# Kernel optimization log

Measured on AMD Instinct MI355X. Metric: run time of the kernel, lower is better.

The kernel has to match this reference:

```python
import jax, jax.numpy as jnp
import numpy as np

DEG = 7
RANK = 8
B = 2_000_000

def setup_inputs() -> dict:
    key = jax.random.key(0)
    k_x, k0, k1, k2, k3 = jax.random.split(key, 5)
    d1 = DEG + 1
    # xavier_normal std = sqrt(2 / (fan_in + fan_out)); for 3D cores torch uses
    # fan_in = rank*(deg+1) style flattening, but any gaussian init is fine for a
    # numerical reference; use std matching 2D xavier on the (first, last) dims.
    def xavier(k, shape):
        fan_in, fan_out = shape[0], shape[-1]
        std = np.sqrt(2.0 / (fan_in + fan_out))
        return jax.random.normal(k, shape, dtype=jnp.float32) * std
    return {
        "X": jax.random.normal(k_x, (B, 4), dtype=jnp.float32),
        "G0": xavier(k0, (d1, RANK)),
        "G1": xavier(k1, (RANK, d1, RANK)),
        "G2": xavier(k2, (RANK, d1, RANK)),
        "G3": xavier(k3, (RANK, d1)),
    }

def reference(X, G0, G1, G2, G3):
    # poly bases: P[b, dim, p] = X[b, dim] ** p, p = 0..deg
    exps = jnp.arange(DEG + 1)               # [d1]
    P = X[:, :, None] ** exps                # [B, 4, d1]
    # chained TT contraction, left to right (avoids any large intermediate)
    t = jnp.einsum('bd,dr->br', P[:, 0], G0)           # [B, r]
    t = jnp.einsum('br,rds,bd->bs', t, G1, P[:, 1])    # [B, r]
    t = jnp.einsum('bs,sdt,bd->bt', t, G2, P[:, 2])    # [B, r]
    res = jnp.einsum('bt,td,bd->b', t, G3, P[:, 3])    # [B]
    return res.reshape(-1, 1)
```

## Files before the change

kernel.cpp:

```cpp
#include <hip/hip_runtime.h>
#include <hip/hip_bf16.h>

typedef float f32x4 __attribute__((ext_vector_type(4)));
typedef short bf16x8 __attribute__((ext_vector_type(8)));

__device__ inline unsigned cvt_pk_bf16(float a, float b) {
    unsigned r;
    asm("v_cvt_pk_bf16_f32 %0, %1, %2" : "=v"(r) : "v"(a), "v"(b));
    return r;
}
union FragU { unsigned u[4]; bf16x8 v; };

__device__ inline bf16x8 pack8(const float f[8]) {
    FragU x;
    x.u[0] = cvt_pk_bf16(f[0], f[1]);
    x.u[1] = cvt_pk_bf16(f[2], f[3]);
    x.u[2] = cvt_pk_bf16(f[4], f[5]);
    x.u[3] = cvt_pk_bf16(f[6], f[7]);
    return x.v;
}

__device__ inline bf16x8 splat8(float v) {
    FragU x;
    unsigned p = cvt_pk_bf16(v, v);
    x.u[0] = p; x.u[1] = p; x.u[2] = p; x.u[3] = p;
    return x.v;
}

__device__ inline void wave_fence() {
    asm volatile("s_waitcnt lgkmcnt(0)" ::: "memory");
    __builtin_amdgcn_sched_barrier(0);
}

__device__ inline void build_b(const float* __restrict__ G, int col, int grp,
                               bf16x8* Bh, bf16x8* Bl) {
    #pragma unroll
    for (int q = 0; q < 2; ++q) {
        FragU hi, lo;
        #pragma unroll
        for (int pr = 0; pr < 4; ++pr) {
            float v0 = 0.f, v1 = 0.f;
            if (col < 8) {
                v0 = G[(32*q + 8*grp + 2*pr    ) * 8 + col];
                v1 = G[(32*q + 8*grp + 2*pr + 1) * 8 + col];
            }
            float h0 = __bfloat162float(__float2bfloat16(v0));
            float h1 = __bfloat162float(__float2bfloat16(v1));
            hi.u[pr] = cvt_pk_bf16(h0, h1);
            lo.u[pr] = cvt_pk_bf16(v0 - h0, v1 - h1);
        }
        Bh[q] = hi.v;
        Bl[q] = lo.v;
    }
}

#define POWERS(p, xx)                                              \
    p[0] = 1.f;  p[1] = (xx);      p[2] = p[1]*p[1];               \
    p[3] = p[2]*p[1]; p[4] = p[2]*p[2]; p[5] = p[4]*p[1];          \
    p[6] = p[4]*p[2]; p[7] = p[4]*p[3];

#define ROWW 12

__global__ __launch_bounds__(256) void tt_poly_kernel(
    const float* __restrict__ X,
    const float* __restrict__ G0,
    const float* __restrict__ G1,
    const float* __restrict__ G2,
    const float* __restrict__ G3,
    float* __restrict__ out,
    int B, int NW)
{
    __shared__ float L[4][3][64 * ROWW];

    const int tid  = threadIdx.x;
    const int w    = tid >> 6;
    const int lane = tid & 63;
    const int col  = lane & 15;
    const int grp  = lane >> 4;

    int rowLbl[4], slotLbl[4], colOk[4];
    {
        bf16x8 ones = splat8(1.f);
        bf16x8 lbl  = splat8((float)col);
        f32x4 pr = {0.f, 0.f, 0.f, 0.f};
        f32x4 pc = {0.f, 0.f, 0.f, 0.f};
        pr = __builtin_amdgcn_mfma_f32_16x16x32_bf16(lbl, ones, pr, 0, 0, 0);
        pc = __builtin_amdgcn_mfma_f32_16x16x32_bf16(ones, lbl, pc, 0, 0, 0);
        #pragma unroll
        for (int j = 0; j < 4; ++j) {
            rowLbl[j] = (int)(pr[j] * 0.03125f + 0.5f);
            int c     = (int)(pc[j] * 0.03125f + 0.5f);
            colOk[j]  = (c < 8);
            slotLbl[j] = 2 * (c & 3) + ((c >> 2) & 1);
        }
    }

    bf16x8 B1h[2], B1l[2], B2h[2], B2l[2];
    build_b(G1, col, grp, B1h, B1l);
    build_b(G2, col, grp, B2h, B2l);

    float* T0 = &L[w][0][0];
    float* T1 = &L[w][1][0];
    float* T2 = &L[w][2][0];
    const int gw = blockIdx.x * 4 + w;

    #pragma unroll 1
    for (int it = 0; it < 4; ++it) {
        const int b = (it * NW + gw) * 64 + lane;
        float4 xv = make_float4(0.f, 0.f, 0.f, 0.f);
        if (b < B) xv = reinterpret_cast<const float4*>(X)[b];

        {
            float p[8];
            POWERS(p, xv.x)
            float t[8];
            #pragma unroll
            for (int r = 0; r < 8; ++r) {
                float a = 0.f;
                #pragma unroll
                for (int d = 0; d < 8; ++d)
                    a = fmaf(p[d], G0[d*8 + r], a);
                t[r] = a;
            }
            f32x4 v0 = {t[0], t[4], t[1], t[5]};
            f32x4 v1 = {t[2], t[6], t[3], t[7]};
            *reinterpret_cast<f32x4*>(&T0[lane*ROWW    ]) = v0;
            *reinterpret_cast<f32x4*>(&T0[lane*ROWW + 4]) = v1;
            *reinterpret_cast<float2*>(&T0[lane*ROWW + 8]) = make_float2(xv.y, xv.z);
        }
        wave_fence();

        #pragma unroll
        for (int g4 = 0; g4 < 4; ++g4) {
            const int base = (g4*16 + col) * ROWW;
            float2 tp = *reinterpret_cast<const float2*>(&T0[base + 2*grp]);
            float x1  = T0[base + 8];
            float p[8];
            POWERS(p, x1)
            float f0[8], f1[8];
            #pragma unroll
            for (int e = 0; e < 8; ++e) { f0[e] = tp.x*p[e]; f1[e] = tp.y*p[e]; }
            bf16x8 a0 = pack8(f0), a1 = pack8(f1);
            f32x4 acc = {0.f, 0.f, 0.f, 0.f};
            acc = __builtin_amdgcn_mfma_f32_16x16x32_bf16(a0, B1h[0], acc, 0, 0, 0);
            acc = __builtin_amdgcn_mfma_f32_16x16x32_bf16(a0, B1l[0], acc, 0, 0, 0);
            acc = __builtin_amdgcn_mfma_f32_16x16x32_bf16(a1, B1h[1], acc, 0, 0, 0);
            acc = __builtin_amdgcn_mfma_f32_16x16x32_bf16(a1, B1l[1], acc, 0, 0, 0);
            #pragma unroll
            for (int j = 0; j < 4; ++j)
                if (colOk[j])
                    T1[(g4*16 + rowLbl[j])*ROWW + slotLbl[j]] = acc[j];
        }
        wave_fence();

        #pragma unroll
        for (int g4 = 0; g4 < 4; ++g4) {
            const int base = (g4*16 + col) * ROWW;
            float2 tp = *reinterpret_cast<const float2*>(&T1[base + 2*grp]);
            float x2  = T0[base + 9];
            float p[8];
            POWERS(p, x2)
            float f0[8], f1[8];
            #pragma unroll
            for (int e = 0; e < 8; ++e) { f0[e] = tp.x*p[e]; f1[e] = tp.y*p[e]; }
            bf16x8 a0 = pack8(f0), a1 = pack8(f1);
            f32x4 acc = {0.f, 0.f, 0.f, 0.f};
            acc = __builtin_amdgcn_mfma_f32_16x16x32_bf16(a0, B2h[0], acc, 0, 0, 0);
            acc = __builtin_amdgcn_mfma_f32_16x16x32_bf16(a0, B2l[0], acc, 0, 0, 0);
            acc = __builtin_amdgcn_mfma_f32_16x16x32_bf16(a1, B2h[1], acc, 0, 0, 0);
            acc = __builtin_amdgcn_mfma_f32_16x16x32_bf16(a1, B2l[1], acc, 0, 0, 0);
            #pragma unroll
            for (int j = 0; j < 4; ++j)
                if (colOk[j])
                    T2[(g4*16 + rowLbl[j])*ROWW + slotLbl[j]] = acc[j];
        }
        wave_fence();

        {
            f32x4 u0 = *reinterpret_cast<const f32x4*>(&T2[lane*ROWW    ]);
            f32x4 u1 = *reinterpret_cast<const f32x4*>(&T2[lane*ROWW + 4]);
            const int tmap[8] = {0, 4, 1, 5, 2, 6, 3, 7};
            float p[8];
            POWERS(p, xv.w)
            float res = 0.f;
            #pragma unroll
            for (int sl = 0; sl < 8; ++sl) {
                const int t8 = tmap[sl];
                float wt = G3[t8*8];
                #pragma unroll
                for (int d = 1; d < 8; ++d)
                    wt = fmaf(p[d], G3[t8*8 + d], wt);
                float tv = (sl < 4) ? u0[sl] : u1[sl - 4];
                res = fmaf(tv, wt, res);
            }
            if (b < B) out[b] = res;
        }
    }
}

extern "C" void kernel_launch(void* const* d_in, const int* in_sizes, int n_in,
                              void* d_out, int out_size, void* d_ws, size_t ws_size,
                              hipStream_t stream) {
    const float* X  = (const float*)d_in[0];
    const float* G0 = (const float*)d_in[1];
    const float* G1 = (const float*)d_in[2];
    const float* G2 = (const float*)d_in[3];
    const float* G3 = (const float*)d_in[4];
    float* out = (float*)d_out;

    int B = in_sizes[0] / 4;
    int block = 256;
    int grid = (B + 1023) / 1024;
    int NW = grid * 4;
    tt_poly_kernel<<<grid, block, 0, stream>>>(X, G0, G1, G2, G3, out, B, NW);
}
```

Measured before the change: 40.37 us.

## Fold G0 into G1 core and restructure LDS staging with vectorized stores

Precomputes G0·G1 into a combined MFMA B operand, so the first contraction builds the x0 powers directly in the A fragment and the per-sample 64-FMA G0 stage and its LDS round trip are gone. LDS intermediates move to a transposed [slot][sample] layout that takes whole f32x4 stores when the MFMA lane mapping matches the expected one, with a scalar fallback otherwise. All four X loads are hoisted ahead of the loop and the loop is fully unrolled to overlap global latency. This costs extra registers and per-block setup FMAs, and the fused core may change rounding in the split-bf16 path.

```diff
diff --git a/kernel.cpp b/kernel.cpp
--- a/kernel.cpp
+++ b/kernel.cpp
@@ -11,7 +11,7 @@
 }
 union FragU { unsigned u[4]; bf16x8 v; };
 
-__device__ inline bf16x8 pack8(const float f[8]) {
+__device__ inline bf16x8 pack8(const float* f) {
     FragU x;
     x.u[0] = cvt_pk_bf16(f[0], f[1]);
     x.u[1] = cvt_pk_bf16(f[2], f[3]);
@@ -19,39 +19,15 @@
     x.u[3] = cvt_pk_bf16(f[6], f[7]);
     return x.v;
 }
-
 __device__ inline bf16x8 splat8(float v) {
     FragU x;
     unsigned p = cvt_pk_bf16(v, v);
     x.u[0] = p; x.u[1] = p; x.u[2] = p; x.u[3] = p;
     return x.v;
 }
-
 __device__ inline void wave_fence() {
     asm volatile("s_waitcnt lgkmcnt(0)" ::: "memory");
     __builtin_amdgcn_sched_barrier(0);
-}
-
-__device__ inline void build_b(const float* __restrict__ G, int col, int grp,
-                               bf16x8* Bh, bf16x8* Bl) {
-    #pragma unroll
-    for (int q = 0; q < 2; ++q) {
-        FragU hi, lo;
-        #pragma unroll
-        for (int pr = 0; pr < 4; ++pr) {
-            float v0 = 0.f, v1 = 0.f;
-            if (col < 8) {
-                v0 = G[(32*q + 8*grp + 2*pr    ) * 8 + col];
-                v1 = G[(32*q + 8*grp + 2*pr + 1) * 8 + col];
-            }
-            float h0 = __bfloat162float(__float2bfloat16(v0));
-            float h1 = __bfloat162float(__float2bfloat16(v1));
-            hi.u[pr] = cvt_pk_bf16(h0, h1);
-            lo.u[pr] = cvt_pk_bf16(v0 - h0, v1 - h1);
-        }
-        Bh[q] = hi.v;
-        Bl[q] = lo.v;
-    }
 }
 
 #define POWERS(p, xx)                                              \
@@ -59,7 +35,7 @@
     p[3] = p[2]*p[1]; p[4] = p[2]*p[2]; p[5] = p[4]*p[1];          \
     p[6] = p[4]*p[2]; p[7] = p[4]*p[3];
 
-#define ROWW 12
+#define TS 72
 
 __global__ __launch_bounds__(256) void tt_poly_kernel(
     const float* __restrict__ X,
@@ -70,15 +46,27 @@
     float* __restrict__ out,
     int B, int NW)
 {
-    __shared__ float L[4][3][64 * ROWW];
+    __shared__ float Xb[4][256];
+    __shared__ float T1s[4][8 * TS];
+    __shared__ float T2s[4][8 * TS];
 
     const int tid  = threadIdx.x;
     const int w    = tid >> 6;
     const int lane = tid & 63;
     const int col  = lane & 15;
     const int grp  = lane >> 4;
-
-    int rowLbl[4], slotLbl[4], colOk[4];
+    const int gw   = blockIdx.x * 4 + w;
+
+    float4 xva[4];
+    #pragma unroll
+    for (int it = 0; it < 4; ++it) {
+        int b = (it * NW + gw) * 64 + lane;
+        xva[it] = (b < B) ? reinterpret_cast<const float4*>(X)[b]
+                          : make_float4(0.f, 0.f, 0.f, 0.f);
+    }
+
+    int rowLbl[4], colLbl[4], rpL[4];
+    bool okl = true;
     {
         bf16x8 ones = splat8(1.f);
         bf16x8 lbl  = splat8((float)col);
@@ -89,109 +77,135 @@
         #pragma unroll
         for (int j = 0; j < 4; ++j) {
             rowLbl[j] = (int)(pr[j] * 0.03125f + 0.5f);
-            int c     = (int)(pc[j] * 0.03125f + 0.5f);
-            colOk[j]  = (c < 8);
-            slotLbl[j] = 2 * (c & 3) + ((c >> 2) & 1);
-        }
-    }
-
-    bf16x8 B1h[2], B1l[2], B2h[2], B2l[2];
-    build_b(G1, col, grp, B1h, B1l);
-    build_b(G2, col, grp, B2h, B2l);
-
-    float* T0 = &L[w][0][0];
-    float* T1 = &L[w][1][0];
-    float* T2 = &L[w][2][0];
-    const int gw = blockIdx.x * 4 + w;
-
-    #pragma unroll 1
+            colLbl[j] = (int)(pc[j] * 0.03125f + 0.5f);
+            rpL[j]    = 2 * (colLbl[j] & 3) + ((colLbl[j] >> 2) & 1);
+            okl = okl && (rowLbl[j] == 4 * grp + j) && (colLbl[j] == col);
+        }
+    }
+    const bool vecok = (__ballot(okl) == ~0ull);
+
+    bf16x8 H1h[2], H1l[2], B2h[2], B2l[2];
+    #pragma unroll
+    for (int q = 0; q < 2; ++q) {
+        float hi[8], lo[8];
+        #pragma unroll
+        for (int j = 0; j < 8; ++j) {
+            float v = 0.f;
+            if (col < 8) {
+                #pragma unroll
+                for (int r = 0; r < 8; ++r)
+                    v = fmaf(G0[(4*q+grp)*8 + r], G1[(r*8 + j)*8 + col], v);
+            }
+            float h = __bfloat162float(__float2bfloat16(v));
+            hi[j] = h; lo[j] = v - h;
+        }
+        H1h[q] = pack8(hi); H1l[q] = pack8(lo);
+    }
+    #pragma unroll
+    for (int q = 0; q < 2; ++q) {
+        float hi[8], lo[8];
+        #pragma unroll
+        for (int j = 0; j < 8; ++j) {
+            float v = (col < 8) ? G2[((4*q+grp)*8 + j)*8 + col] : 0.f;
+            float h = __bfloat162float(__float2bfloat16(v));
+            hi[j] = h; lo[j] = v - h;
+        }
+        B2h[q] = pack8(hi); B2l[q] = pack8(lo);
+    }
+
+    float* Xw  = &Xb[w][0];
+    float* T1w = &T1s[w][0];
+    float* T2w = &T2s[w][0];
+
+    #pragma unroll
     for (int it = 0; it < 4; ++it) {
         const int b = (it * NW + gw) * 64 + lane;
-        float4 xv = make_float4(0.f, 0.f, 0.f, 0.f);
-        if (b < B) xv = reinterpret_cast<const float4*>(X)[b];
-
-        {
-            float p[8];
-            POWERS(p, xv.x)
-            float t[8];
-            #pragma unroll
-            for (int r = 0; r < 8; ++r) {
-                float a = 0.f;
-                #pragma unroll
-                for (int d = 0; d < 8; ++d)
-                    a = fmaf(p[d], G0[d*8 + r], a);
-                t[r] = a;
-            }
-            f32x4 v0 = {t[0], t[4], t[1], t[5]};
-            f32x4 v1 = {t[2], t[6], t[3], t[7]};
-            *reinterpret_cast<f32x4*>(&T0[lane*ROWW    ]) = v0;
-            *reinterpret_cast<f32x4*>(&T0[lane*ROWW + 4]) = v1;
-            *reinterpret_cast<float2*>(&T0[lane*ROWW + 8]) = make_float2(xv.y, xv.z);
-        }
+        const float4 xv = xva[it];
+
+        *reinterpret_cast<f32x4*>(&Xw[lane * 4]) = (f32x4){xv.x, xv.y, xv.z, xv.w};
         wave_fence();
 
+        float x2keep[4];
+
         #pragma unroll
         for (int g4 = 0; g4 < 4; ++g4) {
-            const int base = (g4*16 + col) * ROWW;
-            float2 tp = *reinterpret_cast<const float2*>(&T0[base + 2*grp]);
-            float x1  = T0[base + 8];
-            float p[8];
-            POWERS(p, x1)
+            f32x4 xq = *reinterpret_cast<const f32x4*>(&Xw[(g4*16 + col) * 4]);
+            x2keep[g4] = xq.z;
+            float p1[8];
+            POWERS(p1, xq.y)
+            float x0 = xq.x;
+            float x02 = x0 * x0, x04 = x02 * x02;
+            float e1 = (grp & 1) ? x0  : 1.f;
+            float e2 = (grp & 2) ? x02 : 1.f;
+            float xg = e1 * e2, xg4 = xg * x04;
             float f0[8], f1[8];
             #pragma unroll
-            for (int e = 0; e < 8; ++e) { f0[e] = tp.x*p[e]; f1[e] = tp.y*p[e]; }
+            for (int e = 0; e < 8; ++e) { f0[e] = xg * p1[e]; f1[e] = xg4 * p1[e]; }
             bf16x8 a0 = pack8(f0), a1 = pack8(f1);
             f32x4 acc = {0.f, 0.f, 0.f, 0.f};
-            acc = __builtin_amdgcn_mfma_f32_16x16x32_bf16(a0, B1h[0], acc, 0, 0, 0);
-            acc = __builtin_amdgcn_mfma_f32_16x16x32_bf16(a0, B1l[0], acc, 0, 0, 0);
-            acc = __builtin_amdgcn_mfma_f32_16x16x32_bf16(a1, B1h[1], acc, 0, 0, 0);
-            acc = __builtin_amdgcn_mfma_f32_16x16x32_bf16(a1, B1l[1], acc, 0, 0, 0);
-            #pragma unroll
-            for (int j = 0; j < 4; ++j)
-                if (colOk[j])
-                    T1[(g4*16 + rowLbl[j])*ROWW + slotLbl[j]] = acc[j];
+            acc = __builtin_amdgcn_mfma_f32_16x16x32_bf16(a0, H1h[0], acc, 0, 0, 0);
+            acc = __builtin_amdgcn_mfma_f32_16x16x32_bf16(a0, H1l[0], acc, 0, 0, 0);
+            acc = __builtin_amdgcn_mfma_f32_16x16x32_bf16(a1, H1h[1], acc, 0, 0, 0);
+            acc = __builtin_amdgcn_mfma_f32_16x16x32_bf16(a1, H1l[1], acc, 0, 0, 0);
+            if (vecok) {
+                if (col < 8) {
+                    int rp = 2 * (col & 3) + (col >> 2);
+                    *reinterpret_cast<f32x4*>(&T1w[rp * TS + g4*16 + 4*grp]) = acc;
+                }
+            } else {
+                #pragma unroll
+                for (int j = 0; j < 4; ++j)
+                    if (colLbl[j] < 8)
+                        T1w[rpL[j] * TS + g4*16 + rowLbl[j]] = acc[j];
+            }
         }
         wave_fence();
 
         #pragma unroll
         for (int g4 = 0; g4 < 4; ++g4) {
-            const int base = (g4*16 + col) * ROWW;
-            float2 tp = *reinterpret_cast<const float2*>(&T1[base + 2*grp]);
-            float x2  = T0[base + 9];
-            float p[8];
-            POWERS(p, x2)
+            float t1a = T1w[(2*grp) * TS      + g4*16 + col];
+            float t1b = T1w[(2*grp) * TS + TS + g4*16 + col];
+            float p2[8];
+            POWERS(p2, x2keep[g4])
             float f0[8], f1[8];
             #pragma unroll
-            for (int e = 0; e < 8; ++e) { f0[e] = tp.x*p[e]; f1[e] = tp.y*p[e]; }
+            for (int e = 0; e < 8; ++e) { f0[e] = t1a * p2[e]; f1[e] = t1b * p2[e]; }
             bf16x8 a0 = pack8(f0), a1 = pack8(f1);
             f32x4 acc = {0.f, 0.f, 0.f, 0.f};
             acc = __builtin_amdgcn_mfma_f32_16x16x32_bf16(a0, B2h[0], acc, 0, 0, 0);
             acc = __builtin_amdgcn_mfma_f32_16x16x32_bf16(a0, B2l[0], acc, 0, 0, 0);
             acc = __builtin_amdgcn_mfma_f32_16x16x32_bf16(a1, B2h[1], acc, 0, 0, 0);
             acc = __builtin_amdgcn_mfma_f32_16x16x32_bf16(a1, B2l[1], acc, 0, 0, 0);
-            #pragma unroll
-            for (int j = 0; j < 4; ++j)
-                if (colOk[j])
-                    T2[(g4*16 + rowLbl[j])*ROWW + slotLbl[j]] = acc[j];
+            if (vecok) {
+                if (col < 8) {
+                    int rp = 2 * (col & 3) + (col >> 2);
+                    *reinterpret_cast<f32x4*>(&T2w[rp * TS + g4*16 + 4*grp]) = acc;
+                }
+            } else {
+                #pragma unroll
+                for (int j = 0; j < 4; ++j)
+                    if (colLbl[j] < 8)
+                        T2w[rpL[j] * TS + g4*16 + rowLbl[j]] = acc[j];
+            }
         }
         wave_fence();
 
         {
-            f32x4 u0 = *reinterpret_cast<const f32x4*>(&T2[lane*ROWW    ]);
-            f32x4 u1 = *reinterpret_cast<const f32x4*>(&T2[lane*ROWW + 4]);
-            const int tmap[8] = {0, 4, 1, 5, 2, 6, 3, 7};
-            float p[8];
-            POWERS(p, xv.w)
+            float u[8];
+            #pragma unroll
+            for (int sl = 0; sl < 8; ++sl)
+                u[sl] = T2w[sl * TS + lane];
+            float p3[8];
+            POWERS(p3, xv.w)
             float res = 0.f;
             #pragma unroll
             for (int sl = 0; sl < 8; ++sl) {
-                const int t8 = tmap[sl];
-                float wt = G3[t8*8];
+                const int t8 = (sl & 1) * 4 + (sl >> 1);
+                float wt = G3[t8 * 8];
                 #pragma unroll
                 for (int d = 1; d < 8; ++d)
-                    wt = fmaf(p[d], G3[t8*8 + d], wt);
-                float tv = (sl < 4) ? u0[sl] : u1[sl - 4];
-                res = fmaf(tv, wt, res);
+                    wt = fmaf(p3[d], G3[t8 * 8 + d], wt);
+                res = fmaf(u[sl], wt, res);
             }
             if (b < B) out[b] = res;
         }
```

New measurement: 41.90 us. 3.8% more time.
